# Optimization experiments

Hardware: AMD Instinct MI355X
Metric: run time of the kernel (lower is better)

## Reference

```python
import jax, jax.numpy as jnp
import numpy as np

N_NODES = 100000
N_EDGES = 1600000
IN_FEATS = 128
HIDDEN = 128
OUT_DIM = 128


def setup_inputs() -> dict:
    key = jax.random.key(0)
    ks = jax.random.split(key, 8)
    x = jax.random.normal(ks[0], (N_NODES, IN_FEATS), dtype=jnp.float32)
    W1 = jax.random.normal(ks[1], (IN_FEATS, HIDDEN), dtype=jnp.float32) * (1.0 / np.sqrt(IN_FEATS))
    b1 = jnp.zeros((HIDDEN,), dtype=jnp.float32)
    W2 = jax.random.normal(ks[2], (HIDDEN, HIDDEN), dtype=jnp.float32) * (1.0 / np.sqrt(HIDDEN))
    b2 = jnp.zeros((HIDDEN,), dtype=jnp.float32)
    W3 = jax.random.normal(ks[3], (HIDDEN, OUT_DIM), dtype=jnp.float32) * (1.0 / np.sqrt(HIDDEN))
    b3 = jnp.zeros((OUT_DIM,), dtype=jnp.float32)
    edge_src = jax.random.randint(ks[4], (N_EDGES,), 0, N_NODES, dtype=jnp.int32)
    edge_dst = jax.random.randint(ks[5], (N_EDGES,), 0, N_NODES, dtype=jnp.int32)
    return {"x": x, "W1": W1, "b1": b1, "W2": W2, "b2": b2, "W3": W3, "b3": b3,
            "edge_src": edge_src, "edge_dst": edge_dst}


def _mean_agg(h, edge_src, edge_dst, inv_deg):
    # gather src features, scatter-sum to dst, divide by in-degree (mean)
    summed = jax.ops.segment_sum(h[edge_src], edge_dst, num_segments=N_NODES)
    return summed * inv_deg[:, None]


def reference(x, W1, b1, W2, b2, W3, b3, edge_src, edge_dst):
    # in-degree (clamped to 1 to avoid div-by-zero, matching mean over empty = 0)
    deg = jax.ops.segment_sum(jnp.ones((N_EDGES,), dtype=jnp.float32), edge_dst,
                              num_segments=N_NODES)
    inv_deg = 1.0 / jnp.maximum(deg, 1.0)

    # DGL GINConv (eps=0, mean): h = Linear(h + mean_neighbors(h))
    h = x
    h = (h + _mean_agg(h, edge_src, edge_dst, inv_deg)) @ W1 + b1
    h = jax.nn.relu(h)  # dropout inactive in eval mode
    h = (h + _mean_agg(h, edge_src, edge_dst, inv_deg)) @ W2 + b2
    h = jax.nn.relu(h)
    h = (h + _mean_agg(h, edge_src, edge_dst, inv_deg)) @ W3 + b3
    return h
```

## Files before the change

### kernel.cpp

```cpp
#include <hip/hip_runtime.h>
#include <hip/hip_bf16.h>
#include <stdint.h>

#if __has_builtin(__builtin_amdgcn_cvt_pk_f32_fp8) && __has_builtin(__builtin_amdgcn_cvt_pk_fp8_f32)
#define FP8_HW 1
#else
#define FP8_HW 0
#include <hip/hip_fp8.h>
#endif

#define N_NODES 100000
#define N_EDGES 1600000
#define FEAT 128

#define BKT_SHIFT 8
#define BKT_SIZE  256
#define NB_BKT    391
#define BKT_CAP   4864
#define NB_A      400
#define EPB       4000

typedef uint16_t u16;
typedef uint32_t u32;
typedef __attribute__((ext_vector_type(8))) short bf16x8;
typedef __attribute__((ext_vector_type(4))) float f32x4;
typedef __attribute__((ext_vector_type(2))) float f32x2;

__device__ __forceinline__ u16 bf16_rn(float f){
  u32 u = __float_as_uint(f);
  u += 0x7FFFu + ((u >> 16) & 1u);
  return (u16)(u >> 16);
}
__device__ __forceinline__ float bf16_lo(u32 p){ return __uint_as_float(p << 16); }
__device__ __forceinline__ float bf16_hi(u32 p){ return __uint_as_float(p & 0xFFFF0000u); }

__device__ __forceinline__ void fp8x4_to_f32(u32 w, float* o){
#if FP8_HW
  f32x2 a = __builtin_amdgcn_cvt_pk_f32_fp8(w, false);
  f32x2 b = __builtin_amdgcn_cvt_pk_f32_fp8(w, true);
  o[0] = a.x; o[1] = a.y; o[2] = b.x; o[3] = b.y;
#else
  #pragma unroll
  for (int i = 0; i < 4; ++i){
    __hip_fp8_e4m3 t; t.__x = (uint8_t)((w >> (8 * i)) & 0xFF);
    o[i] = (float)t;
  }
#endif
}
__device__ __forceinline__ u32 f32x4_to_fp8(float a, float b, float c, float d){
#if FP8_HW
  u32 r = __builtin_amdgcn_cvt_pk_fp8_f32(a, b, 0, false);
  r = __builtin_amdgcn_cvt_pk_fp8_f32(c, d, r, true);
  return r;
#else
  __hip_fp8_e4m3 qa(a), qb(b), qc(c), qd(d);
  return (u32)qa.__x | ((u32)qb.__x << 8) | ((u32)qc.__x << 16) | ((u32)qd.__x << 24);
#endif
}


__global__ void bucket_scatter_kernel(const int* __restrict__ src, const int* __restrict__ dst,
                                      int* __restrict__ cursor, uint2* __restrict__ bbuf){
  __shared__ int h[NB_BKT];
  __shared__ int res[NB_BKT];
  for (int i = threadIdx.x; i < NB_BKT; i += 256) h[i] = 0;
  __syncthreads();
  int base = blockIdx.x * EPB;
  int end  = min(base + EPB, N_EDGES);
  for (int e = base + threadIdx.x; e < end; e += 256)
    atomicAdd(&h[dst[e] >> BKT_SHIFT], 1);
  __syncthreads();
  for (int i = threadIdx.x; i < NB_BKT; i += 256){
    int c = h[i];
    res[i] = c ? atomicAdd(&cursor[i], c) : 0;
    h[i] = 0;
  }
  __syncthreads();
  for (int e = base + threadIdx.x; e < end; e += 256){
    int d = dst[e];
    int b = d >> BKT_SHIFT;
    int p = atomicAdd(&h[b], 1);
    bbuf[(size_t)b * BKT_CAP + res[b] + p] = make_uint2((u32)src[e], (u32)(d & (BKT_SIZE - 1)));
  }
}

__global__ void csr_build_kernel(const uint2* __restrict__ bbuf, const int* __restrict__ cursor,
                                 int* __restrict__ offs, int* __restrict__ deg,
                                 float* __restrict__ inv_deg, int* __restrict__ eidx){
  __shared__ int hist[BKT_SIZE];
  __shared__ int s[BKT_SIZE];
  __shared__ int cu[BKT_SIZE];
  int b = blockIdx.x;
  int t = threadIdx.x;
  int lo = b * BKT_CAP;
  int hi = lo + cursor[b];
  hist[t] = 0;
  __syncthreads();
  for (int e = lo + t; e < hi; e += BKT_SIZE)
    atomicAdd(&hist[bbuf[e].y], 1);
  __syncthreads();
  int v  = hist[t];
  int pv = (v + 3) & ~3;
  s[t] = pv;
  __syncthreads();
  for (int d = 1; d < BKT_SIZE; d <<= 1){
    int u = (t >= d) ? s[t - d] : 0;
    __syncthreads();
    s[t] += u;
    __syncthreads();
  }
  int excl = s[t] - pv;
  int node = b * BKT_SIZE + t;
  if (node < N_NODES){
    offs[node]    = lo + excl;
    deg[node]     = v;
    inv_deg[node] = 1.0f / fmaxf((float)v, 1.0f);
  }
  __syncthreads();
  s[t]  = excl;
  cu[t] = 0;
  __syncthreads();
  for (int e = lo + t; e < hi; e += BKT_SIZE){
    uint2 q = bbuf[e];
    int p = atomicAdd(&cu[q.y], 1);
    eidx[lo + s[q.y] + p] = (int)q.x;
  }
}


__global__ void cvt_x8_kernel(const float* __restrict__ x, uint2* __restrict__ X8){
  int i = blockIdx.x * 256 + threadIdx.x;
  const float4* p = (const float4*)x + (size_t)i * 2;
  float4 a = p[0], b = p[1];
  uint2 o;
  o.x = f32x4_to_fp8(a.x, a.y, a.z, a.w);
  o.y = f32x4_to_fp8(b.x, b.y, b.z, b.w);
  X8[i] = o;
}

__global__ void cvt_h8_kernel(const u16* __restrict__ H, uint2* __restrict__ H8){
  int i = blockIdx.x * 256 + threadIdx.x;
  uint4 hq = ((const uint4*)H)[i];
  uint2 o;
  o.x = f32x4_to_fp8(bf16_lo(hq.x), bf16_hi(hq.x), bf16_lo(hq.y), bf16_hi(hq.y));
  o.y = f32x4_to_fp8(bf16_lo(hq.z), bf16_hi(hq.z), bf16_lo(hq.w), bf16_hi(hq.w));
  H8[i] = o;
}

__global__ void wprep3_kernel(const float* __restrict__ W1, const float* __restrict__ W2,
                              const float* __restrict__ W3, u16* __restrict__ Wp1,
                              u16* __restrict__ Wp2, u16* __restrict__ Wp3){
  int which = blockIdx.x >> 6;
  int b     = blockIdx.x & 63;
  const float* W = (which == 0) ? W1 : (which == 1) ? W2 : W3;
  u16*        Wp = (which == 0) ? Wp1 : (which == 1) ? Wp2 : Wp3;
  int idx = b * 256 + threadIdx.x;
  int j    = idx & 7;
  int lane = (idx >> 3) & 63;
  int t    = idx >> 9;
  int k0 = t & 3, n0 = t >> 2;
  int k = k0 * 32 + (lane >> 4) * 8 + j;
  int n = n0 * 16 + (lane & 15);
  Wp[idx] = bf16_rn(W[k * FEAT + n]);
}

template<int SM>
__global__ void agg16_kernel(const u32* __restrict__ n8,
                             const u16* __restrict__ hb,
                             const float* __restrict__ xf,
                             const int* __restrict__ offs,
                             const int* __restrict__ deg,
                             const float* __restrict__ inv_deg,
                             const int* __restrict__ eidx,
                             u16* __restrict__ T){
  int wid   = (int)((blockIdx.x * 256u + threadIdx.x) >> 6);
  int lane  = threadIdx.x & 63;
  int nsub  = lane >> 4;
  int slice = lane & 15;
  int node  = wid * 4 + nsub;
  bool vn   = node < N_NODES;
  int nc    = vn ? node : 0;
  int start = offs[nc];
  int cnt   = vn ? deg[nc] : 0;
  const int* ep = eidx + start;

  float acc[8];
  #pragma unroll
  for (int j = 0; j < 8; ++j) acc[j] = 0.f;

  uint4 q = (cnt > 0) ? *(const uint4*)ep : make_uint4(0, 0, 0, 0);

  for (int e = 0; e < cnt; e += 4){
    uint4 qn = *(const uint4*)(ep + e + 4);
    int i0 = (int)q.x, i1 = (int)q.y, i2 = (int)q.z, i3 = (int)q.w;
    float f0 = 1.f;
    float f1 = (e + 1 < cnt) ? 1.f : 0.f; if (e + 1 >= cnt) i1 = 0;
    float f2 = (e + 2 < cnt) ? 1.f : 0.f; if (e + 2 >= cnt) i2 = 0;
    float f3 = (e + 3 < cnt) ? 1.f : 0.f; if (e + 3 >= cnt) i3 = 0;
    uint2 r0 = *(const uint2*)(n8 + (size_t)i0 * 32 + slice * 2);
    uint2 r1 = *(const uint2*)(n8 + (size_t)i1 * 32 + slice * 2);
    uint2 r2 = *(const uint2*)(n8 + (size_t)i2 * 32 + slice * 2);
    uint2 r3 = *(const uint2*)(n8 + (size_t)i3 * 32 + slice * 2);
    float t0[4], t1[4];
    fp8x4_to_f32(r0.x, t0); fp8x4_to_f32(r0.y, t1);
    acc[0]+=f0*t0[0]; acc[1]+=f0*t0[1]; acc[2]+=f0*t0[2]; acc[3]+=f0*t0[3];
    acc[4]+=f0*t1[0]; acc[5]+=f0*t1[1]; acc[6]+=f0*t1[2]; acc[7]+=f0*t1[3];
    fp8x4_to_f32(r1.x, t0); fp8x4_to_f32(r1.y, t1);
    acc[0]+=f1*t0[0]; acc[1]+=f1*t0[1]; acc[2]+=f1*t0[2]; acc[3]+=f1*t0[3];
    acc[4]+=f1*t1[0]; acc[5]+=f1*t1[1]; acc[6]+=f1*t1[2]; acc[7]+=f1*t1[3];
    fp8x4_to_f32(r2.x, t0); fp8x4_to_f32(r2.y, t1);
    acc[0]+=f2*t0[0]; acc[1]+=f2*t0[1]; acc[2]+=f2*t0[2]; acc[3]+=f2*t0[3];
    acc[4]+=f2*t1[0]; acc[5]+=f2*t1[1]; acc[6]+=f2*t1[2]; acc[7]+=f2*t1[3];
    fp8x4_to_f32(r3.x, t0); fp8x4_to_f32(r3.y, t1);
    acc[0]+=f3*t0[0]; acc[1]+=f3*t0[1]; acc[2]+=f3*t0[2]; acc[3]+=f3*t0[3];
    acc[4]+=f3*t1[0]; acc[5]+=f3*t1[1]; acc[6]+=f3*t1[2]; acc[7]+=f3*t1[3];
    q = qn;
  }

  if (!vn) return;
  float w = inv_deg[node];
  float self[8];
  if (SM == 1){
    const float* sp = xf + (size_t)node * FEAT + slice * 8;
    float4 a = *(const float4*)sp;
    float4 b = *(const float4*)(sp + 4);
    self[0]=a.x; self[1]=a.y; self[2]=a.z; self[3]=a.w;
    self[4]=b.x; self[5]=b.y; self[6]=b.z; self[7]=b.w;
  } else {
    const u16* sp = hb + (size_t)node * FEAT + slice * 8;
    uint4 s0 = *(const uint4*)sp;
    self[0]=bf16_lo(s0.x); self[1]=bf16_hi(s0.x); self[2]=bf16_lo(s0.y); self[3]=bf16_hi(s0.y);
    self[4]=bf16_lo(s0.z); self[5]=bf16_hi(s0.z); self[6]=bf16_lo(s0.w); self[7]=bf16_hi(s0.w);
  }
  uint4 o;
  o.x = (u32)bf16_rn(self[0] + w*acc[0]) | ((u32)bf16_rn(self[1] + w*acc[1]) << 16);
  o.y = (u32)bf16_rn(self[2] + w*acc[2]) | ((u32)bf16_rn(self[3] + w*acc[3]) << 16);
  o.z = (u32)bf16_rn(self[4] + w*acc[4]) | ((u32)bf16_rn(self[5] + w*acc[5]) << 16);
  o.w = (u32)bf16_rn(self[6] + w*acc[6]) | ((u32)bf16_rn(self[7] + w*acc[7]) << 16);
  *(uint4*)(T + (size_t)node * FEAT + slice * 8) = o;
}

template<int MODE>
__global__ __launch_bounds__(256) void gemm2_kernel(const u16* __restrict__ T,
                                                    const u16* __restrict__ Wp,
                                                    const float* __restrict__ bias,
                                                    void* __restrict__ out){
  int wave = threadIdx.x >> 6;
  int lane = threadIdx.x & 63;
  int row0 = blockIdx.x * 128 + wave * 32;
  if (row0 >= N_NODES) return;
  int quad = lane >> 4;
  int c    = lane & 15;

  f32x4 acc[2][8];
  #pragma unroll
  for (int t = 0; t < 2; ++t)
    #pragma unroll
    for (int i = 0; i < 8; ++i) acc[t][i] = (f32x4){0.f, 0.f, 0.f, 0.f};

  bf16x8 A[2][4];
  const u16* ar0 = T + (size_t)(row0 + c) * FEAT + quad * 8;
  const u16* ar1 = ar0 + 16 * FEAT;
  #pragma unroll
  for (int k0 = 0; k0 < 4; ++k0){
    A[0][k0] = *(const bf16x8*)(ar0 + k0 * 32);
    A[1][k0] = *(const bf16x8*)(ar1 + k0 * 32);
  }

  #pragma unroll
  for (int n0 = 0; n0 < 8; ++n0){
    #pragma unroll
    for (int k0 = 0; k0 < 4; ++k0){
      bf16x8 b = *(const bf16x8*)(Wp + (((n0 << 2) | k0) * 64 + lane) * 8);
      acc[0][n0] = __builtin_amdgcn_mfma_f32_16x16x32_bf16(A[0][k0], b, acc[0][n0], 0, 0, 0);
      acc[1][n0] = __builtin_amdgcn_mfma_f32_16x16x32_bf16(A[1][k0], b, acc[1][n0], 0, 0, 0);
    }
  }

  #pragma unroll
  for (int t = 0; t < 2; ++t){
    #pragma unroll
    for (int n0 = 0; n0 < 8; ++n0){
      float bv = bias[n0 * 16 + c];
      #pragma unroll
      for (int r = 0; r < 4; ++r){
        int row = row0 + t * 16 + quad * 4 + r;
        int col = n0 * 16 + c;
        float v = acc[t][n0][r] + bv;
        if (MODE == 0){
          v = fmaxf(v, 0.f);
          ((u16*)out)[(size_t)row * FEAT + col] = bf16_rn(v);
        } else {
          ((float*)out)[(size_t)row * FEAT + col] = v;
        }
      }
    }
  }
}


static inline size_t align_up(size_t x){ return (x + 255) & ~(size_t)255; }

extern "C" void kernel_launch(void* const* d_in, const int* in_sizes, int n_in,
                              void* d_out, int out_size, void* d_ws, size_t ws_size,
                              hipStream_t stream){
  const float* x  = (const float*)d_in[0];
  const float* W1 = (const float*)d_in[1];
  const float* b1 = (const float*)d_in[2];
  const float* W2 = (const float*)d_in[3];
  const float* b2 = (const float*)d_in[4];
  const float* W3 = (const float*)d_in[5];
  const float* b3 = (const float*)d_in[6];
  const int* esrc = (const int*)d_in[7];
  const int* edst = (const int*)d_in[8];

  char* w = (char*)d_ws;
  int*   cursor  = (int*)w;    w += align_up((size_t)NB_BKT * 4);
  int*   deg     = (int*)w;    w += align_up((size_t)N_NODES * 4);
  int*   offs    = (int*)w;    w += align_up((size_t)N_NODES * 4);
  float* inv_deg = (float*)w;  w += align_up((size_t)N_NODES * 4);
  int*   eidx    = (int*)w;    w += align_up((size_t)NB_BKT * BKT_CAP * 4);
  u16*   Wp1     = (u16*)w;    w += align_up((size_t)16384 * 2);
  u16*   Wp2     = (u16*)w;    w += align_up((size_t)16384 * 2);
  u16*   Wp3     = (u16*)w;    w += align_up((size_t)16384 * 2);
  u16*   T       = (u16*)w;    w += align_up((size_t)N_NODES * FEAT * 2);

  uint2* bbuf = (uint2*)T;

  u16* H  = (u16*)d_out;
  u32* H8 = (u32*)((char*)d_out + (size_t)N_NODES * FEAT * 2);
  u32* X8 = (u32*)((char*)d_out + (size_t)N_NODES * FEAT * 3);

  hipMemsetAsync(cursor, 0, (size_t)NB_BKT * 4, stream);

  bucket_scatter_kernel<<<NB_A, 256, 0, stream>>>(esrc, edst, cursor, bbuf);
  csr_build_kernel<<<NB_BKT, BKT_SIZE, 0, stream>>>(bbuf, cursor, offs, deg, inv_deg, eidx);

  wprep3_kernel<<<192, 256, 0, stream>>>(W1, W2, W3, Wp1, Wp2, Wp3);
  cvt_x8_kernel<<<N_EDGES / 256, 256, 0, stream>>>(x, (uint2*)X8);

  const int AGG_BLOCKS  = (N_NODES + 15) / 16;
  const int GEMM_BLOCKS = (N_NODES + 127) / 128;
  const int CVT_BLOCKS  = N_EDGES / 256;

  agg16_kernel<1><<<AGG_BLOCKS, 256, 0, stream>>>(X8, (const u16*)nullptr, x,
                                                  offs, deg, inv_deg, eidx, T);
  gemm2_kernel<0><<<GEMM_BLOCKS, 256, 0, stream>>>(T, Wp1, b1, H);

  cvt_h8_kernel<<<CVT_BLOCKS, 256, 0, stream>>>(H, (uint2*)H8);
  agg16_kernel<0><<<AGG_BLOCKS, 256, 0, stream>>>(H8, H, (const float*)nullptr,
                                                  offs, deg, inv_deg, eidx, T);
  gemm2_kernel<0><<<GEMM_BLOCKS, 256, 0, stream>>>(T, Wp2, b2, H);

  cvt_h8_kernel<<<CVT_BLOCKS, 256, 0, stream>>>(H, (uint2*)H8);
  agg16_kernel<0><<<AGG_BLOCKS, 256, 0, stream>>>(H8, H, (const float*)nullptr,
                                                  offs, deg, inv_deg, eidx, T);
  gemm2_kernel<1><<<GEMM_BLOCKS, 256, 0, stream>>>(T, Wp3, b3, d_out);

  (void)in_sizes; (void)n_in; (void)out_size; (void)ws_size; (void)w;
}
```

Baseline: 340.2 us.

## Replace block-local bucket scatter with per-edge global atomics and widen CSR build blocks

The bucket scatter drops its two-pass shared-memory histogram and reservation scheme. Each edge now does one global atomicAdd on its bucket cursor, with one thread per edge across many more blocks. The CSR build kernel now runs 1024 threads per block, so each bucket's edges are processed with four times the parallelism. The change cuts the phases and barriers in the scatter, but it adds heavy global atomic contention on 391 counters and raises the bucket capacity to cover less-local ordering.

```diff
diff --git a/kernel.cpp b/kernel.cpp
--- a/kernel.cpp
+++ b/kernel.cpp
@@ -16,9 +16,7 @@
 #define BKT_SHIFT 8
 #define BKT_SIZE  256
 #define NB_BKT    391
-#define BKT_CAP   4864
-#define NB_A      400
-#define EPB       4000
+#define BKT_CAP   5120
 
 typedef uint16_t u16;
 typedef uint32_t u32;
@@ -61,30 +59,16 @@
 
 __global__ void bucket_scatter_kernel(const int* __restrict__ src, const int* __restrict__ dst,
                                       int* __restrict__ cursor, uint2* __restrict__ bbuf){
-  __shared__ int h[NB_BKT];
-  __shared__ int res[NB_BKT];
-  for (int i = threadIdx.x; i < NB_BKT; i += 256) h[i] = 0;
-  __syncthreads();
-  int base = blockIdx.x * EPB;
-  int end  = min(base + EPB, N_EDGES);
-  for (int e = base + threadIdx.x; e < end; e += 256)
-    atomicAdd(&h[dst[e] >> BKT_SHIFT], 1);
-  __syncthreads();
-  for (int i = threadIdx.x; i < NB_BKT; i += 256){
-    int c = h[i];
-    res[i] = c ? atomicAdd(&cursor[i], c) : 0;
-    h[i] = 0;
-  }
-  __syncthreads();
-  for (int e = base + threadIdx.x; e < end; e += 256){
-    int d = dst[e];
-    int b = d >> BKT_SHIFT;
-    int p = atomicAdd(&h[b], 1);
-    bbuf[(size_t)b * BKT_CAP + res[b] + p] = make_uint2((u32)src[e], (u32)(d & (BKT_SIZE - 1)));
-  }
-}
-
-__global__ void csr_build_kernel(const uint2* __restrict__ bbuf, const int* __restrict__ cursor,
+  int e = blockIdx.x * 256 + threadIdx.x;
+  if (e >= N_EDGES) return;
+  int d = dst[e];
+  int b = d >> BKT_SHIFT;
+  int p = atomicAdd(&cursor[b], 1);
+  bbuf[(size_t)b * BKT_CAP + p] = make_uint2((u32)src[e], (u32)(d & (BKT_SIZE - 1)));
+}
+
+__global__ __launch_bounds__(1024) void csr_build_kernel(const uint2* __restrict__ bbuf,
+                                 const int* __restrict__ cursor,
                                  int* __restrict__ offs, int* __restrict__ deg,
                                  float* __restrict__ inv_deg, int* __restrict__ eidx){
   __shared__ int hist[BKT_SIZE];
@@ -94,33 +78,37 @@
   int t = threadIdx.x;
   int lo = b * BKT_CAP;
   int hi = lo + cursor[b];
-  hist[t] = 0;
+  if (t < BKT_SIZE) hist[t] = 0;
   __syncthreads();
-  for (int e = lo + t; e < hi; e += BKT_SIZE)
+  for (int e = lo + t; e < hi; e += 1024)
     atomicAdd(&hist[bbuf[e].y], 1);
   __syncthreads();
-  int v  = hist[t];
-  int pv = (v + 3) & ~3;
-  s[t] = pv;
+  int v = 0, pv = 0;
+  if (t < BKT_SIZE){
+    v  = hist[t];
+    pv = (v + 3) & ~3;
+    s[t] = pv;
+  }
   __syncthreads();
   for (int d = 1; d < BKT_SIZE; d <<= 1){
-    int u = (t >= d) ? s[t - d] : 0;
+    int add = (t < BKT_SIZE && t >= d) ? s[t - d] : 0;
     __syncthreads();
-    s[t] += u;
+    if (t < BKT_SIZE && t >= d) s[t] += add;
     __syncthreads();
   }
-  int excl = s[t] - pv;
-  int node = b * BKT_SIZE + t;
-  if (node < N_NODES){
-    offs[node]    = lo + excl;
-    deg[node]     = v;
-    inv_deg[node] = 1.0f / fmaxf((float)v, 1.0f);
+  if (t < BKT_SIZE){
+    int excl = s[t] - pv;
+    int node = b * BKT_SIZE + t;
+    if (node < N_NODES){
+      offs[node]    = lo + excl;
+      deg[node]     = v;
+      inv_deg[node] = 1.0f / fmaxf((float)v, 1.0f);
+    }
+    s[t]  = excl;
+    cu[t] = 0;
   }
   __syncthreads();
-  s[t]  = excl;
-  cu[t] = 0;
-  __syncthreads();
-  for (int e = lo + t; e < hi; e += BKT_SIZE){
+  for (int e = lo + t; e < hi; e += 1024){
     uint2 q = bbuf[e];
     int p = atomicAdd(&cu[q.y], 1);
     eidx[lo + s[q.y] + p] = (int)q.x;
@@ -333,8 +321,8 @@
 
   hipMemsetAsync(cursor, 0, (size_t)NB_BKT * 4, stream);
 
-  bucket_scatter_kernel<<<NB_A, 256, 0, stream>>>(esrc, edst, cursor, bbuf);
-  csr_build_kernel<<<NB_BKT, BKT_SIZE, 0, stream>>>(bbuf, cursor, offs, deg, inv_deg, eidx);
+  bucket_scatter_kernel<<<(N_EDGES + 255) / 256, 256, 0, stream>>>(esrc, edst, cursor, bbuf);
+  csr_build_kernel<<<NB_BKT, 1024, 0, stream>>>(bbuf, cursor, offs, deg, inv_deg, eidx);
 
   wprep3_kernel<<<192, 256, 0, stream>>>(W1, W2, W3, Wp1, Wp2, Wp3);
   cvt_x8_kernel<<<N_EDGES / 256, 256, 0, stream>>>(x, (uint2*)X8);
```

Measured after the change: 869.0 us. 155% more time.
